# Kernel tuning notes

Hardware: AMD Instinct MI355X
Metric: run time of the kernel (lower is better)

The kernel has to match this reference:

```python
import jax, jax.numpy as jnp
import numpy as np

NUM_HEADS = 16
MAX_ITERATIONS = 4
EPSILON = 3.0
MOMENTUM = 0.2
ENTROPY_PENALTY = 0.05


def setup_inputs() -> dict:
    key = jax.random.key(0)
    ks = jax.random.split(key, 6)
    B, S, D = 2, 1024, 1024
    scale = 0.02
    return {
        "x": jax.random.normal(ks[0], (B, S, D), dtype=jnp.float32),
        "wq": jax.random.normal(ks[1], (D, D), dtype=jnp.float32) * scale,
        "bq": jnp.zeros((D,), dtype=jnp.float32),
        "wk": jax.random.normal(ks[2], (D, D), dtype=jnp.float32) * scale,
        "bk": jnp.zeros((D,), dtype=jnp.float32),
        "wv": jax.random.normal(ks[3], (D, D), dtype=jnp.float32) * scale,
        "bv": jnp.zeros((D,), dtype=jnp.float32),
        "wo": jax.random.normal(ks[4], (D, D), dtype=jnp.float32) * scale,
        "bo": jnp.zeros((D,), dtype=jnp.float32),
        "res_bias": jnp.zeros((1, NUM_HEADS, 1, 1), dtype=jnp.float32),
    }


def _entropy(attn):
    # attn: [B, H, S, S] -> [B, H]; matches compute_entropy (chunking is math-neutral)
    p = attn + 1e-10
    return (-jnp.sum(p * jnp.log(p), axis=-1)).mean(axis=-1)


def reference(x, wq, bq, wk, bk, wv, bv, wo, bo, res_bias):
    B, S, D = x.shape
    H = NUM_HEADS
    hd = D // H
    # projections (torch Linear: y = x @ W^T + b)
    q = (x @ wq.T + bq).reshape(B, S, H, hd).transpose(0, 2, 1, 3)
    k = (x @ wk.T + bk).reshape(B, S, H, hd).transpose(0, 2, 1, 3)
    v = (x @ wv.T + bv).reshape(B, S, H, hd).transpose(0, 2, 1, 3)

    # scores are loop-invariant in the source (q, k never change inside the loop)
    scores = jnp.einsum("bhqd,bhkd->bhqk", q, k) / jnp.float32(hd) ** 0.5
    scores = scores + res_bias
    cur = jax.nn.softmax(scores, axis=-1)  # [B, H, S, S]

    # iteration 0
    attn = cur
    prev_attn = jax.lax.stop_gradient(attn)
    ent = _entropy(attn)                       # [B, H]
    prev_ent = jax.lax.stop_gradient(ent)
    iters = jnp.array(1, dtype=jnp.int32)
    done = jnp.all(ent.mean(axis=1) < EPSILON)  # scalar bool (torch breaks on .all())

    for t in range(1, MAX_ITERATIONS):
        blended = (1.0 - MOMENTUM) * cur + MOMENTUM * prev_attn
        new_attn = blended / blended.sum(axis=-1, keepdims=True)
        attn = jnp.where(done, attn, new_attn)
        prev_attn = jax.lax.stop_gradient(attn)

        new_ent = _entropy(attn)
        # entropy-increase penalty (per batch element)
        inc = new_ent.mean(axis=1) > prev_ent.mean(axis=1)  # [B]
        new_ent = jnp.where(inc[:, None],
                            new_ent * (1.0 - ENTROPY_PENALTY) + prev_ent * ENTROPY_PENALTY,
                            new_ent)
        ent = jnp.where(done, ent, new_ent)
        prev_ent = jax.lax.stop_gradient(ent)

        iters = jnp.where(done, iters, jnp.int32(t + 1))
        done = done | jnp.all(ent.mean(axis=1) < EPSILON)

    # output is recomputed each torch iteration but only the last survives
    attn_out = jnp.einsum("bhqk,bhkd->bhqd", attn, v)
    attn_out = attn_out.transpose(0, 2, 1, 3).reshape(B, S, D)
    out = attn_out @ wo.T + bo
    return (out, ent, iters)
```

## Files before the change

### kernel.cpp

```cpp
#include <hip/hip_runtime.h>
#include <hip/hip_bf16.h>

typedef __attribute__((ext_vector_type(4))) float f32x4;
typedef __attribute__((ext_vector_type(8))) __bf16 bf16x8;
typedef __attribute__((ext_vector_type(8))) unsigned short ushort8;

__device__ __forceinline__ unsigned short f2bf(float f) {
    unsigned u = __builtin_bit_cast(unsigned, f);
    unsigned lsb = (u >> 16) & 1u;
    u += 0x7fffu + lsb;
    return (unsigned short)(u >> 16);
}

__device__ __forceinline__ f32x4 mfma16(ushort8 a, ushort8 b, f32x4 c) {
    return __builtin_amdgcn_mfma_f32_16x16x32_bf16(
        __builtin_bit_cast(bf16x8, a), __builtin_bit_cast(bf16x8, b), c, 0, 0, 0);
}

__device__ __forceinline__ void gload_lds16(const unsigned short* g, unsigned short* l) {
    __builtin_amdgcn_global_load_lds(
        (const __attribute__((address_space(1))) unsigned int*)g,
        (__attribute__((address_space(3))) unsigned int*)l, 16, 0, 0);
}

__global__ __launch_bounds__(256) void cvt_all_kernel(
    const float* __restrict__ x, const float* __restrict__ wq, const float* __restrict__ wk,
    const float* __restrict__ wv, const float* __restrict__ wo, unsigned short* __restrict__ dst) {
    int i = blockIdx.x * blockDim.x + threadIdx.x;
    const float* src;
    size_t off;
    if (i < 524288) { src = x; off = i; }
    else {
        int j = i - 524288;
        int w = j >> 18;
        off = (size_t)(j & 262143);
        src = (w == 0) ? wq : (w == 1) ? wk : (w == 2) ? wv : wo;
    }
    float4 v = ((const float4*)src)[off];
    ushort4 o;
    o.x = f2bf(v.x); o.y = f2bf(v.y); o.z = f2bf(v.z); o.w = f2bf(v.w);
    ((ushort4*)dst)[i] = o;
}

__global__ __launch_bounds__(256) void gemm_qkv(
    const unsigned short* __restrict__ xb,
    const unsigned short* __restrict__ wqb, const unsigned short* __restrict__ wkb,
    const unsigned short* __restrict__ wvb,
    const float* __restrict__ bq, const float* __restrict__ bk, const float* __restrict__ bv,
    unsigned short* __restrict__ qo, unsigned short* __restrict__ ko, unsigned short* __restrict__ vt) {
    const int N = 1024, K = 1024;
    int flat = blockIdx.x + 16 * blockIdx.y + 256 * blockIdx.z;
    int vid = (flat & 7) * 96 + (flat >> 3);
    int bx = vid & 15, by = (vid >> 4) & 15, bz = vid >> 8;
    const unsigned short* Bt = (bz == 0) ? wqb : (bz == 1) ? wkb : wvb;
    const float* bias = (bz == 0) ? bq : (bz == 1) ? bk : bv;

    __shared__ unsigned short As[2][128 * 64];
    __shared__ unsigned short Bs[2][64 * 64];
    int tid = threadIdx.x;
    int wave = tid >> 6, lane = tid & 63;
    int lr = lane & 15, lk = lane >> 4;
    int m0 = bx * 128, n0 = by * 64;
    int wr = wave >> 1, wc = wave & 1;

    f32x4 acc[4][2] = {};

    auto stage = [&](int p, int kk) {
#pragma unroll
        for (int i = 0; i < 4; ++i) {
            int c = tid + 256 * i;
            int r = c >> 3, s = c & 7;
            gload_lds16(xb + (size_t)(m0 + r) * K + kk + (s ^ (r & 7)) * 8, &As[p][c * 8]);
        }
#pragma unroll
        for (int i = 0; i < 2; ++i) {
            int c = tid + 256 * i;
            int r = c >> 3, s = c & 7;
            gload_lds16(Bt + (size_t)(n0 + r) * K + kk + (s ^ (r & 7)) * 8, &Bs[p][c * 8]);
        }
    };

    stage(0, 0);
    asm volatile("s_waitcnt vmcnt(0)" ::: "memory");
    __syncthreads();

    for (int t = 0; t < 16; ++t) {
        int p = t & 1;
        if (t < 15) stage(p ^ 1, (t + 1) * 64);
#pragma unroll
        for (int ks = 0; ks < 2; ++ks) {
            ushort8 af[4], bfr[2];
#pragma unroll
            for (int f = 0; f < 4; ++f) {
                int row = wr * 64 + f * 16 + lr;
                int cc = ks * 4 + lk;
                af[f] = *(const ushort8*)&As[p][row * 64 + ((cc ^ (row & 7)) * 8)];
            }
#pragma unroll
            for (int f = 0; f < 2; ++f) {
                int row = wc * 32 + f * 16 + lr;
                int cc = ks * 4 + lk;
                bfr[f] = *(const ushort8*)&Bs[p][row * 64 + ((cc ^ (row & 7)) * 8)];
            }
#pragma unroll
            for (int i = 0; i < 4; ++i)
#pragma unroll
                for (int j = 0; j < 2; ++j)
                    acc[i][j] = mfma16(af[i], bfr[j], acc[i][j]);
        }
        __syncthreads();
    }

    if (bz < 2) {
        unsigned short* C = (bz == 0) ? qo : ko;
#pragma unroll
        for (int i = 0; i < 4; ++i)
#pragma unroll
            for (int j = 0; j < 2; ++j)
#pragma unroll
                for (int r = 0; r < 4; ++r) {
                    int row = m0 + wr * 64 + i * 16 + lk * 4 + r;
                    int col = n0 + wc * 32 + j * 16 + lr;
                    C[(size_t)row * N + col] = f2bf(acc[i][j][r] + bias[col]);
                }
    } else {
#pragma unroll
        for (int i = 0; i < 4; ++i)
#pragma unroll
            for (int j = 0; j < 2; ++j) {
                int row = m0 + wr * 64 + i * 16 + lk * 4;
                int col = n0 + wc * 32 + j * 16 + lr;
                int b = row >> 10, n = row & 1023;
                float bb = bias[col];
                ushort4 o4;
                o4.x = f2bf(acc[i][j][0] + bb);
                o4.y = f2bf(acc[i][j][1] + bb);
                o4.z = f2bf(acc[i][j][2] + bb);
                o4.w = f2bf(acc[i][j][3] + bb);
                *(ushort4*)&vt[((size_t)(b * 16 + (col >> 6)) * 64 + (col & 63)) * 1024 + n] = o4;
            }
    }
}

__global__ __launch_bounds__(256) void gemm_out(
    const unsigned short* __restrict__ Ab, const unsigned short* __restrict__ Btb,
    const float* __restrict__ bias, float* __restrict__ C,
    const float* __restrict__ ent_part, float* __restrict__ out_ent,
    float* __restrict__ out_iters) {
    const int N = 1024, K = 1024;
    int flat = blockIdx.x + 16 * blockIdx.y;
    int vid = (flat & 7) * 32 + (flat >> 3);
    int bx = vid & 15, by = vid >> 4;
    int tid = threadIdx.x;
    int wave = tid >> 6, lane = tid & 63;

    if (flat == 0 && wave == 0) {
        float s = 0.f;
        if (lane < 32) {
            for (int i = 0; i < 16; ++i) s += ent_part[lane * 16 + i];
            s *= (1.0f / 1024.0f);
            out_ent[lane] = s;
        }
        float m = s;
        m += __shfl_xor(m, 1, 64); m += __shfl_xor(m, 2, 64);
        m += __shfl_xor(m, 4, 64); m += __shfl_xor(m, 8, 64);
        float m1 = __shfl(m, 16, 64);
        if (lane == 0) {
            float e0 = m * (1.f / 16.f), e1 = m1 * (1.f / 16.f);
            out_iters[0] = (e0 < 3.0f && e1 < 3.0f) ? 1.0f : 4.0f;
        }
    }

    __shared__ unsigned short As[2][128 * 64];
    __shared__ unsigned short Bs[2][64 * 64];
    int lr = lane & 15, lk = lane >> 4;
    int m0 = bx * 128, n0 = by * 64;
    int wr = wave >> 1, wc = wave & 1;

    f32x4 acc[4][2] = {};

    auto stage = [&](int p, int kk) {
#pragma unroll
        for (int i = 0; i < 4; ++i) {
            int c = tid + 256 * i;
            int r = c >> 3, s = c & 7;
            gload_lds16(Ab + (size_t)(m0 + r) * K + kk + (s ^ (r & 7)) * 8, &As[p][c * 8]);
        }
#pragma unroll
        for (int i = 0; i < 2; ++i) {
            int c = tid + 256 * i;
            int r = c >> 3, s = c & 7;
            gload_lds16(Btb + (size_t)(n0 + r) * K + kk + (s ^ (r & 7)) * 8, &Bs[p][c * 8]);
        }
    };

    stage(0, 0);
    asm volatile("s_waitcnt vmcnt(0)" ::: "memory");
    __syncthreads();

    for (int t = 0; t < 16; ++t) {
        int p = t & 1;
        if (t < 15) stage(p ^ 1, (t + 1) * 64);
#pragma unroll
        for (int ks = 0; ks < 2; ++ks) {
            ushort8 af[4], bfr[2];
#pragma unroll
            for (int f = 0; f < 4; ++f) {
                int row = wr * 64 + f * 16 + lr;
                int cc = ks * 4 + lk;
                af[f] = *(const ushort8*)&As[p][row * 64 + ((cc ^ (row & 7)) * 8)];
            }
#pragma unroll
            for (int f = 0; f < 2; ++f) {
                int row = wc * 32 + f * 16 + lr;
                int cc = ks * 4 + lk;
                bfr[f] = *(const ushort8*)&Bs[p][row * 64 + ((cc ^ (row & 7)) * 8)];
            }
#pragma unroll
            for (int i = 0; i < 4; ++i)
#pragma unroll
                for (int j = 0; j < 2; ++j)
                    acc[i][j] = mfma16(af[i], bfr[j], acc[i][j]);
        }
        __syncthreads();
    }

#pragma unroll
    for (int i = 0; i < 4; ++i)
#pragma unroll
        for (int j = 0; j < 2; ++j)
#pragma unroll
            for (int r = 0; r < 4; ++r) {
                int row = m0 + wr * 64 + i * 16 + lk * 4 + r;
                int col = n0 + wc * 32 + j * 16 + lr;
                C[(size_t)row * N + col] = acc[i][j][r] + bias[col];
            }
}

__global__ __launch_bounds__(256) void attn_kernel(
    const unsigned short* __restrict__ qb, const unsigned short* __restrict__ kb,
    const unsigned short* __restrict__ vtb, const float* __restrict__ res_bias,
    unsigned short* __restrict__ attn_out, float* __restrict__ ent_part) {
    const int S = 1024, D = 1024;
    int flat = blockIdx.x + 16 * blockIdx.y;
    int vid = (flat & 7) * 64 + (flat >> 3);
    int qt = vid & 15;
    int bh = vid >> 4;
    int b = bh >> 4, h = bh & 15;
    int tid = threadIdx.x;
    int wave = tid >> 6, lane = tid & 63;
    int lr = lane & 15, lk = lane >> 4;

    __shared__ unsigned short Ks[128 * 64];
    __shared__ unsigned short Vts[64 * 128];
    __shared__ unsigned short Ps[64 * 128];
    __shared__ float wpart[4];

    const float rb = res_bias[h];
    const unsigned short* qg = qb + (size_t)(b * S + qt * 64) * D + h * 64;
    const unsigned short* kg = kb + (size_t)(b * S) * D + h * 64;
    const unsigned short* vtg = vtb + (size_t)bh * 64 * 1024;

    ushort8 qf[2];
#pragma unroll
    for (int ks = 0; ks < 2; ++ks)
        qf[ks] = *(const ushort8*)(qg + (size_t)(wave * 16 + lr) * D + (ks * 4 + lk) * 8);

    ushort8 kr[4], vr[4];
#pragma unroll
    for (int i = 0; i < 4; ++i) {
        int c = tid + 256 * i;
        kr[i] = *(const ushort8*)(kg + (size_t)(c >> 3) * D + (c & 7) * 8);
        vr[i] = *(const ushort8*)(vtg + (size_t)(c >> 4) * 1024 + (c & 15) * 8);
    }

    f32x4 o[4] = {};
    float l_ = 0.f, ps_ = 0.f;

    for (int kt = 0; kt < 8; ++kt) {
        __syncthreads();
#pragma unroll
        for (int i = 0; i < 4; ++i) {
            int c = tid + 256 * i;
            int r1 = c >> 3, d1 = c & 7;
            *(ushort8*)&Ks[r1 * 64 + ((d1 ^ (r1 & 7)) * 8)] = kr[i];
            int r2 = c >> 4, d2 = c & 15;
            *(ushort8*)&Vts[r2 * 128 + ((d2 ^ (r2 & 7)) * 8)] = vr[i];
        }
        __syncthreads();

        if (kt < 7) {
#pragma unroll
            for (int i = 0; i < 4; ++i) {
                int c = tid + 256 * i;
                kr[i] = *(const ushort8*)(kg + (size_t)((kt + 1) * 128 + (c >> 3)) * D + (c & 7) * 8);
                vr[i] = *(const ushort8*)(vtg + (size_t)(c >> 4) * 1024 + (kt + 1) * 128 + (c & 15) * 8);
            }
        }

        f32x4 sf[8] = {};
        __builtin_amdgcn_s_setprio(1);
#pragma unroll
        for (int ks = 0; ks < 2; ++ks) {
#pragma unroll
            for (int fj = 0; fj < 8; ++fj) {
                ushort8 kf = *(const ushort8*)&Ks[(fj * 16 + lr) * 64 + (((ks * 4 + lk) ^ (lr & 7)) * 8)];
                sf[fj] = mfma16(kf, qf[ks], sf[fj]);
            }
        }
        __builtin_amdgcn_s_setprio(0);

        float pl = 0.f, ps = 0.f;
#pragma unroll
        for (int fj = 0; fj < 8; ++fj)
#pragma unroll
            for (int r = 0; r < 4; ++r) {
                float sv = sf[fj][r] * 0.125f + rb;
                float p = __expf(sv);
                pl += p; ps += p * sv;
                sf[fj][r] = p;
            }
        int q = wave * 16 + lr;
#pragma unroll
        for (int fj = 0; fj < 8; ++fj) {
            ushort4 pk4;
            pk4.x = f2bf(sf[fj][0]); pk4.y = f2bf(sf[fj][1]);
            pk4.z = f2bf(sf[fj][2]); pk4.w = f2bf(sf[fj][3]);
            *(ushort4*)&Ps[q * 128 + ((fj ^ (lr & 7)) << 4) + (lk << 2)] = pk4;
        }
        pl += __shfl_xor(pl, 16, 64); pl += __shfl_xor(pl, 32, 64);
        ps += __shfl_xor(ps, 16, 64); ps += __shfl_xor(ps, 32, 64);
        l_ += pl; ps_ += ps;

        asm volatile("s_waitcnt lgkmcnt(0)" ::: "memory");
        __builtin_amdgcn_sched_barrier(0);

        __builtin_amdgcn_s_setprio(1);
#pragma unroll
        for (int ks = 0; ks < 4; ++ks) {
            int ch = (ks * 2 + (lk >> 1)) ^ (lr & 7);
            ushort8 ap = *(const ushort8*)&Ps[q * 128 + (ch << 4) + ((lk & 1) << 3)];
#pragma unroll
            for (int fd = 0; fd < 4; ++fd) {
                ushort8 bv8 = *(const ushort8*)&Vts[(fd * 16 + lr) * 128 + (((ks * 4 + lk) ^ (lr & 7)) * 8)];
                o[fd] = mfma16(ap, bv8, o[fd]);
            }
        }
        __builtin_amdgcn_s_setprio(0);
    }

    float linv = 1.f / l_;
    float ent_row = __logf(l_) - ps_ * linv;
    float linv_r[4];
#pragma unroll
    for (int r = 0; r < 4; ++r) linv_r[r] = __shfl(linv, lk * 4 + r, 64);
#pragma unroll
    for (int r = 0; r < 4; ++r) {
        int row = b * S + qt * 64 + wave * 16 + lk * 4 + r;
#pragma unroll
        for (int fd = 0; fd < 4; ++fd) {
            int col = h * 64 + fd * 16 + lr;
            attn_out[(size_t)row * D + col] = f2bf(o[fd][r] * linv_r[r]);
        }
    }
    float es = ent_row;
    es += __shfl_xor(es, 1, 64);
    es += __shfl_xor(es, 2, 64);
    es += __shfl_xor(es, 4, 64);
    es += __shfl_xor(es, 8, 64);
    if (lane == 0) wpart[wave] = es;
    __syncthreads();
    if (tid == 0) ent_part[bh * 16 + qt] = wpart[0] + wpart[1] + wpart[2] + wpart[3];
}

extern "C" void kernel_launch(void* const* d_in, const int* in_sizes, int n_in,
                              void* d_out, int out_size, void* d_ws, size_t ws_size,
                              hipStream_t stream) {
    const float* x  = (const float*)d_in[0];
    const float* wq = (const float*)d_in[1];
    const float* bq = (const float*)d_in[2];
    const float* wk = (const float*)d_in[3];
    const float* bk = (const float*)d_in[4];
    const float* wv = (const float*)d_in[5];
    const float* bv = (const float*)d_in[6];
    const float* wo = (const float*)d_in[7];
    const float* bo = (const float*)d_in[8];
    const float* rbias = (const float*)d_in[9];

    char* ws = (char*)d_ws;
    unsigned short* xb  = (unsigned short*)(ws);
    unsigned short* wqb = (unsigned short*)(ws + ((size_t)4 << 20));
    unsigned short* wkb = (unsigned short*)(ws + ((size_t)6 << 20));
    unsigned short* wvb = (unsigned short*)(ws + ((size_t)8 << 20));
    unsigned short* wob = (unsigned short*)(ws + ((size_t)10 << 20));
    unsigned short* qbf = (unsigned short*)(ws + ((size_t)12 << 20));
    unsigned short* kbf = (unsigned short*)(ws + ((size_t)16 << 20));
    unsigned short* vtb = (unsigned short*)(ws + ((size_t)20 << 20));
    unsigned short* aob = (unsigned short*)(ws + ((size_t)24 << 20));
    float* ent_part = (float*)(ws + ((size_t)28 << 20));

    float* out = (float*)d_out;
    float* out_ent = out + (size_t)2 * 1024 * 1024;
    float* out_iters = out_ent + 32;

    cvt_all_kernel<<<dim3(6144), dim3(256), 0, stream>>>(x, wq, wk, wv, wo, xb);
    gemm_qkv<<<dim3(16, 16, 3), dim3(256), 0, stream>>>(xb, wqb, wkb, wvb, bq, bk, bv, qbf, kbf, vtb);
    attn_kernel<<<dim3(16, 32), dim3(256), 0, stream>>>(qbf, kbf, vtb, rbias, aob, ent_part);
    gemm_out<<<dim3(16, 16), dim3(256), 0, stream>>>(aob, wob, bo, out, ent_part, out_ent, out_iters);
}
```

Measured before the change: 69.75 us.

## Load V fragments directly to registers, use exp2 and packed bf16 conversion

Removes the V^T shared-memory tile so each wave loads its V operand fragments straight from global memory into registers for the PV MFMAs. This drops the LDS writes and reads for V and one LDS buffer, but the loads are issued inside the loop without prefetching and raise register pressure. The softmax exponent is rewritten to use exp2 with pre-scaled constants, with entropy corrected by ln2. The bf16 packing uses the hardware v_cvt_pk_bf16_f32 instruction.

After: 84.49 us. +21.1%, slower.

```diff
diff --git a/kernel.cpp b/kernel.cpp
--- a/kernel.cpp
+++ b/kernel.cpp
@@ -10,6 +10,12 @@
     unsigned lsb = (u >> 16) & 1u;
     u += 0x7fffu + lsb;
     return (unsigned short)(u >> 16);
+}
+
+__device__ __forceinline__ unsigned cvt_pk_bf16(float lo, float hi) {
+    unsigned r;
+    asm("v_cvt_pk_bf16_f32 %0, %1, %2" : "=v"(r) : "v"(lo), "v"(hi));
+    return r;
 }
 
 __device__ __forceinline__ f32x4 mfma16(ushort8 a, ushort8 b, f32x4 c) {
@@ -242,6 +248,8 @@
     const unsigned short* __restrict__ vtb, const float* __restrict__ res_bias,
     unsigned short* __restrict__ attn_out, float* __restrict__ ent_part) {
     const int S = 1024, D = 1024;
+    const float LOG2E = 1.4426950408889634f;
+    const float LN2 = 0.6931471805599453f;
     int flat = blockIdx.x + 16 * blockIdx.y;
     int vid = (flat & 7) * 64 + (flat >> 3);
     int qt = vid & 15;
@@ -252,11 +260,11 @@
     int lr = lane & 15, lk = lane >> 4;
 
     __shared__ unsigned short Ks[128 * 64];
-    __shared__ unsigned short Vts[64 * 128];
     __shared__ unsigned short Ps[64 * 128];
     __shared__ float wpart[4];
 
-    const float rb = res_bias[h];
+    const float rbl = res_bias[h] * LOG2E;
+    const float c1 = 0.125f * LOG2E;
     const unsigned short* qg = qb + (size_t)(b * S + qt * 64) * D + h * 64;
     const unsigned short* kg = kb + (size_t)(b * S) * D + h * 64;
     const unsigned short* vtg = vtb + (size_t)bh * 64 * 1024;
@@ -266,12 +274,11 @@
     for (int ks = 0; ks < 2; ++ks)
         qf[ks] = *(const ushort8*)(qg + (size_t)(wave * 16 + lr) * D + (ks * 4 + lk) * 8);
 
-    ushort8 kr[4], vr[4];
+    ushort8 kr[4];
 #pragma unroll
     for (int i = 0; i < 4; ++i) {
         int c = tid + 256 * i;
         kr[i] = *(const ushort8*)(kg + (size_t)(c >> 3) * D + (c & 7) * 8);
-        vr[i] = *(const ushort8*)(vtg + (size_t)(c >> 4) * 1024 + (c & 15) * 8);
     }
 
     f32x4 o[4] = {};
@@ -284,17 +291,22 @@
             int c = tid + 256 * i;
             int r1 = c >> 3, d1 = c & 7;
             *(ushort8*)&Ks[r1 * 64 + ((d1 ^ (r1 & 7)) * 8)] = kr[i];
-            int r2 = c >> 4, d2 = c & 15;
-            *(ushort8*)&Vts[r2 * 128 + ((d2 ^ (r2 & 7)) * 8)] = vr[i];
         }
         __syncthreads();
+
+        ushort8 vf[16];
+#pragma unroll
+        for (int ks = 0; ks < 4; ++ks)
+#pragma unroll
+            for (int fd = 0; fd < 4; ++fd)
+                vf[ks * 4 + fd] = *(const ushort8*)(vtg + (size_t)(fd * 16 + lr) * 1024
+                                                    + kt * 128 + (ks * 4 + lk) * 8);
 
         if (kt < 7) {
 #pragma unroll
             for (int i = 0; i < 4; ++i) {
                 int c = tid + 256 * i;
                 kr[i] = *(const ushort8*)(kg + (size_t)((kt + 1) * 128 + (c >> 3)) * D + (c & 7) * 8);
-                vr[i] = *(const ushort8*)(vtg + (size_t)(c >> 4) * 1024 + (kt + 1) * 128 + (c & 15) * 8);
             }
         }
 
@@ -315,18 +327,18 @@
         for (int fj = 0; fj < 8; ++fj)
 #pragma unroll
             for (int r = 0; r < 4; ++r) {
-                float sv = sf[fj][r] * 0.125f + rb;
-                float p = __expf(sv);
-                pl += p; ps += p * sv;
+                float t = sf[fj][r] * c1 + rbl;
+                float p = __builtin_amdgcn_exp2f(t);
+                pl += p; ps = fmaf(p, t, ps);
                 sf[fj][r] = p;
             }
         int q = wave * 16 + lr;
 #pragma unroll
         for (int fj = 0; fj < 8; ++fj) {
-            ushort4 pk4;
-            pk4.x = f2bf(sf[fj][0]); pk4.y = f2bf(sf[fj][1]);
-            pk4.z = f2bf(sf[fj][2]); pk4.w = f2bf(sf[fj][3]);
-            *(ushort4*)&Ps[q * 128 + ((fj ^ (lr & 7)) << 4) + (lk << 2)] = pk4;
+            uint2 pk;
+            pk.x = cvt_pk_bf16(sf[fj][0], sf[fj][1]);
+            pk.y = cvt_pk_bf16(sf[fj][2], sf[fj][3]);
+            *(uint2*)&Ps[q * 128 + ((fj ^ (lr & 7)) << 4) + (lk << 2)] = pk;
         }
         pl += __shfl_xor(pl, 16, 64); pl += __shfl_xor(pl, 32, 64);
         ps += __shfl_xor(ps, 16, 64); ps += __shfl_xor(ps, 32, 64);
@@ -341,16 +353,14 @@
             int ch = (ks * 2 + (lk >> 1)) ^ (lr & 7);
             ushort8 ap = *(const ushort8*)&Ps[q * 128 + (ch << 4) + ((lk & 1) << 3)];
 #pragma unroll
-            for (int fd = 0; fd < 4; ++fd) {
-                ushort8 bv8 = *(const ushort8*)&Vts[(fd * 16 + lr) * 128 + (((ks * 4 + lk) ^ (lr & 7)) * 8)];
-                o[fd] = mfma16(ap, bv8, o[fd]);
-            }
+            for (int fd = 0; fd < 4; ++fd)
+                o[fd] = mfma16(ap, vf[ks * 4 + fd], o[fd]);
         }
         __builtin_amdgcn_s_setprio(0);
     }
 
     float linv = 1.f / l_;
-    float ent_row = __logf(l_) - ps_ * linv;
+    float ent_row = __logf(l_) - LN2 * ps_ * linv;
     float linv_r[4];
 #pragma unroll
     for (int r = 0; r < 4; ++r) linv_r[r] = __shfl(linv, lk * 4 + r, 64);
```

## Double-buffer K/V tiles in LDS and switch softmax to exp2

Applied to the files above, without the earlier changes.

The attention kernel now keeps two LDS buffers for the K and V^T tiles. The next tile is written to the spare buffer while the current one is consumed, which cuts the per-iteration barriers from two to one and prefetches two tiles ahead in registers. The exponential is computed with the native exp2 on log2e-prescaled scores, and the entropy term is corrected by ln2. The cost is more LDS per block (about 80KB instead of 48KB), which may lower how many blocks fit on a CU.

After: 77.24 us. 10.7% more time.

```diff
diff --git a/kernel.cpp b/kernel.cpp
--- a/kernel.cpp
+++ b/kernel.cpp
@@ -242,6 +242,8 @@
     const unsigned short* __restrict__ vtb, const float* __restrict__ res_bias,
     unsigned short* __restrict__ attn_out, float* __restrict__ ent_part) {
     const int S = 1024, D = 1024;
+    const float LOG2E = 1.4426950408889634f;
+    const float LN2 = 0.6931471805599453f;
     int flat = blockIdx.x + 16 * blockIdx.y;
     int vid = (flat & 7) * 64 + (flat >> 3);
     int qt = vid & 15;
@@ -251,12 +253,13 @@
     int wave = tid >> 6, lane = tid & 63;
     int lr = lane & 15, lk = lane >> 4;
 
-    __shared__ unsigned short Ks[128 * 64];
-    __shared__ unsigned short Vts[64 * 128];
+    __shared__ unsigned short Ks[2][128 * 64];
+    __shared__ unsigned short Vts[2][64 * 128];
     __shared__ unsigned short Ps[64 * 128];
     __shared__ float wpart[4];
 
-    const float rb = res_bias[h];
+    const float rbl = res_bias[h] * LOG2E;
+    const float c1 = 0.125f * LOG2E;
     const unsigned short* qg = qb + (size_t)(b * S + qt * 64) * D + h * 64;
     const unsigned short* kg = kb + (size_t)(b * S) * D + h * 64;
     const unsigned short* vtg = vtb + (size_t)bh * 64 * 1024;
@@ -266,37 +269,42 @@
     for (int ks = 0; ks < 2; ++ks)
         qf[ks] = *(const ushort8*)(qg + (size_t)(wave * 16 + lr) * D + (ks * 4 + lk) * 8);
 
+    int ck[4], cv[4];
+#pragma unroll
+    for (int i = 0; i < 4; ++i) { ck[i] = tid + 256 * i; cv[i] = tid + 256 * i; }
+
+    auto load_tile = [&](int kt, ushort8* kr, ushort8* vr) {
+#pragma unroll
+        for (int i = 0; i < 4; ++i) {
+            int c = ck[i];
+            kr[i] = *(const ushort8*)(kg + (size_t)(kt * 128 + (c >> 3)) * D + (c & 7) * 8);
+            vr[i] = *(const ushort8*)(vtg + (size_t)(c >> 4) * 1024 + kt * 128 + (c & 15) * 8);
+        }
+    };
+    auto write_tile = [&](int p, const ushort8* kr, const ushort8* vr) {
+#pragma unroll
+        for (int i = 0; i < 4; ++i) {
+            int c = ck[i];
+            int r1 = c >> 3, d1 = c & 7;
+            *(ushort8*)&Ks[p][r1 * 64 + ((d1 ^ (r1 & 7)) * 8)] = kr[i];
+            int r2 = c >> 4, d2 = c & 15;
+            *(ushort8*)&Vts[p][r2 * 128 + ((d2 ^ (r2 & 7)) * 8)] = vr[i];
+        }
+    };
+
     ushort8 kr[4], vr[4];
-#pragma unroll
-    for (int i = 0; i < 4; ++i) {
-        int c = tid + 256 * i;
-        kr[i] = *(const ushort8*)(kg + (size_t)(c >> 3) * D + (c & 7) * 8);
-        vr[i] = *(const ushort8*)(vtg + (size_t)(c >> 4) * 1024 + (c & 15) * 8);
-    }
+    load_tile(0, kr, vr);
+    write_tile(0, kr, vr);
+    load_tile(1, kr, vr);
+    __syncthreads();
 
     f32x4 o[4] = {};
     float l_ = 0.f, ps_ = 0.f;
 
     for (int kt = 0; kt < 8; ++kt) {
-        __syncthreads();
-#pragma unroll
-        for (int i = 0; i < 4; ++i) {
-            int c = tid + 256 * i;
-            int r1 = c >> 3, d1 = c & 7;
-            *(ushort8*)&Ks[r1 * 64 + ((d1 ^ (r1 & 7)) * 8)] = kr[i];
-            int r2 = c >> 4, d2 = c & 15;
-            *(ushort8*)&Vts[r2 * 128 + ((d2 ^ (r2 & 7)) * 8)] = vr[i];
-        }
-        __syncthreads();
-
-        if (kt < 7) {
-#pragma unroll
-            for (int i = 0; i < 4; ++i) {
-                int c = tid + 256 * i;
-                kr[i] = *(const ushort8*)(kg + (size_t)((kt + 1) * 128 + (c >> 3)) * D + (c & 7) * 8);
-                vr[i] = *(const ushort8*)(vtg + (size_t)(c >> 4) * 1024 + (kt + 1) * 128 + (c & 15) * 8);
-            }
-        }
+        int p = kt & 1;
+        if (kt < 7) write_tile(p ^ 1, kr, vr);
+        if (kt < 6) load_tile(kt + 2, kr, vr);
 
         f32x4 sf[8] = {};
         __builtin_amdgcn_s_setprio(1);
@@ -304,7 +312,7 @@
         for (int ks = 0; ks < 2; ++ks) {
 #pragma unroll
             for (int fj = 0; fj < 8; ++fj) {
-                ushort8 kf = *(const ushort8*)&Ks[(fj * 16 + lr) * 64 + (((ks * 4 + lk) ^ (lr & 7)) * 8)];
+                ushort8 kf = *(const ushort8*)&Ks[p][(fj * 16 + lr) * 64 + (((ks * 4 + lk) ^ (lr & 7)) * 8)];
                 sf[fj] = mfma16(kf, qf[ks], sf[fj]);
             }
         }
@@ -315,10 +323,10 @@
         for (int fj = 0; fj < 8; ++fj)
 #pragma unroll
             for (int r = 0; r < 4; ++r) {
-                float sv = sf[fj][r] * 0.125f + rb;
-                float p = __expf(sv);
-                pl += p; ps += p * sv;
-                sf[fj][r] = p;
+                float t = sf[fj][r] * c1 + rbl;
+                float pe = __builtin_amdgcn_exp2f(t);
+                pl += pe; ps = fmaf(pe, t, ps);
+                sf[fj][r] = pe;
             }
         int q = wave * 16 + lr;
 #pragma unroll
@@ -342,15 +350,16 @@
             ushort8 ap = *(const ushort8*)&Ps[q * 128 + (ch << 4) + ((lk & 1) << 3)];
 #pragma unroll
             for (int fd = 0; fd < 4; ++fd) {
-                ushort8 bv8 = *(const ushort8*)&Vts[(fd * 16 + lr) * 128 + (((ks * 4 + lk) ^ (lr & 7)) * 8)];
+                ushort8 bv8 = *(const ushort8*)&Vts[p][(fd * 16 + lr) * 128 + (((ks * 4 + lk) ^ (lr & 7)) * 8)];
                 o[fd] = mfma16(ap, bv8, o[fd]);
             }
         }
         __builtin_amdgcn_s_setprio(0);
+        __syncthreads();
     }
 
     float linv = 1.f / l_;
-    float ent_row = __logf(l_) - ps_ * linv;
+    float ent_row = __logf(l_) - LN2 * ps_ * linv;
     float linv_r[4];
 #pragma unroll
     for (int r = 0; r < 4; ++r) linv_r[r] = __shfl(linv, lk * 4 + r, 64);
```
